# Performance work log

Hardware: AMD Instinct MI355X
Metric: run time of the kernel (lower is better)

The kernel has to match this reference:

```python
import jax, jax.numpy as jnp
import numpy as np

TEMP = 1.0
B, FLAT, K, D = 8, 262144, 256, 4  # FLAT = M*D, M = 65536


def setup_inputs() -> dict:
    key = jax.random.key(0)
    k1, k2 = jax.random.split(key)
    x = jax.random.normal(k1, (B, FLAT), dtype=jnp.float32)
    center = jax.random.normal(k2, (K, D), dtype=jnp.float32)
    return {"x": x, "center": center}


def reference(x, center):
    # Soft vector quantization (Q_type='Soft')
    x_ = x.reshape(x.shape[0], -1, D)                      # [B, M, 4]
    # sim = -||x - c||^2, expanded to avoid [B,M,K,4] intermediate
    x_sq = jnp.sum(x_ * x_, axis=-1, keepdims=True)        # [B, M, 1]
    c_sq = jnp.sum(center * center, axis=-1)               # [K]
    xc = jnp.einsum('bmd,kd->bmk', x_, center)             # [B, M, K]
    sim = -(x_sq - 2.0 * xc + c_sq)                        # [B, M, K]
    smx = jax.nn.softmax(TEMP * sim, axis=-1)              # [B, M, K]
    output = jnp.einsum('bmk,kd->bmd', smx, center)        # [B, M, 4]
    return output.reshape(x.shape)
```

## Files before the change

### kernel.cpp

```cpp
#include <hip/hip_runtime.h>
#include <hip/hip_bf16.h>

#ifndef __has_builtin
#define __has_builtin(x) 0
#endif

typedef __attribute__((ext_vector_type(8))) short short8;
typedef __attribute__((ext_vector_type(4))) float floatx4;

__device__ __forceinline__ float fast_exp2(float x) {
#if __has_builtin(__builtin_amdgcn_exp2f)
    return __builtin_amdgcn_exp2f(x);
#else
    return exp2f(x);
#endif
}
__device__ __forceinline__ float fast_rcp(float x) {
#if __has_builtin(__builtin_amdgcn_rcpf)
    return __builtin_amdgcn_rcpf(x);
#else
    return 1.0f / x;
#endif
}
__device__ __forceinline__ unsigned pack_bf16(float a, float b) {
    __hip_bfloat162 h = __float22bfloat162_rn(make_float2(a, b));
    union { __hip_bfloat162 h2; unsigned u; } cv;
    cv.h2 = h;
    return cv.u;
}

#define VQ_K 256
#define BLK  256
#define T    4

__global__ __launch_bounds__(BLK, 8) void vq_mfma(const float* __restrict__ x,
                                                  const float* __restrict__ center,
                                                  float* __restrict__ out) {
    __shared__ float    s_c2[2056];
    __shared__ float    s_b[VQ_K];
    __shared__ unsigned s_v[8 * 64 * 4];

    {
        const float L2E = 1.4426950408889634f;
        int k = threadIdx.x;
        float4 c = reinterpret_cast<const float4*>(center)[k];
        float b = -L2E * (c.x * c.x + c.y * c.y + c.z * c.z + c.w * c.w);
        int off = k * 8 + ((k >> 3) & 3) * 4;
        float s = 2.0f * L2E;
        s_c2[off + 0] = s * c.x;
        s_c2[off + 1] = s * c.y;
        s_c2[off + 2] = s * c.z;
        s_c2[off + 3] = s * c.w;
        s_b[k] = b;
    }
    for (int f = threadIdx.x; f < 512; f += BLK) {
        int chunk = f >> 6, ln = f & 63;
        int n = ln & 15, q = ln >> 4;
#pragma unroll
        for (int r = 0; r < 4; ++r) {
            int k0 = chunk * 32 + q * 8 + 2 * r;
            float v0 = (n < 4) ? center[k0 * 4 + n]       : (n == 4 ? 1.f : 0.f);
            float v1 = (n < 4) ? center[(k0 + 1) * 4 + n] : (n == 4 ? 1.f : 0.f);
            s_v[f * 4 + r] = pack_bf16(v0, v1);
        }
    }
    __syncthreads();

    const int lane = threadIdx.x & 63;
    const int wv   = threadIdx.x >> 6;
    const int q    = lane >> 4;
    const int ml   = lane & 15;

    const int mbase = blockIdx.x * (4 * 16 * T) + wv * (16 * T);
    const float4* __restrict__ x4 = reinterpret_cast<const float4*>(x);

    float4 xr[T];
#pragma unroll
    for (int t = 0; t < T; ++t) xr[t] = x4[mbase + t * 16 + ml];

    floatx4 O[T];
#pragma unroll
    for (int t = 0; t < T; ++t) O[t] = (floatx4){0.f, 0.f, 0.f, 0.f};

    union AFrag { unsigned u[4]; short8 v; };

    for (int chunk = 0; chunk < 8; ++chunk) {
        AFrag areg[T];
#pragma unroll
        for (int jj = 0; jj < 4; ++jj) {
            int k0 = chunk * 32 + q * 8 + 2 * jj;
            int o0 = k0 * 8 + q * 4;
            float4 c2a = *reinterpret_cast<const float4*>(s_c2 + o0);
            float4 c2b = *reinterpret_cast<const float4*>(s_c2 + o0 + 8);
            float  ba  = s_b[k0];
            float  bb  = s_b[k0 + 1];
#pragma unroll
            for (int t = 0; t < T; ++t) {
                float s0 = fmaf(xr[t].x, c2a.x, ba);
                s0 = fmaf(xr[t].y, c2a.y, s0);
                s0 = fmaf(xr[t].z, c2a.z, s0);
                s0 = fmaf(xr[t].w, c2a.w, s0);
                float s1 = fmaf(xr[t].x, c2b.x, bb);
                s1 = fmaf(xr[t].y, c2b.y, s1);
                s1 = fmaf(xr[t].z, c2b.z, s1);
                s1 = fmaf(xr[t].w, c2b.w, s1);
                areg[t].u[jj] = pack_bf16(fast_exp2(s0), fast_exp2(s1));
            }
        }
        short8 bfrag = reinterpret_cast<const short8*>(s_v)[chunk * 64 + lane];
#pragma unroll
        for (int t = 0; t < T; ++t) {
            O[t] = __builtin_amdgcn_mfma_f32_16x16x32_bf16(areg[t].v, bfrag,
                                                           O[t], 0, 0, 0);
        }
    }

#pragma unroll
    for (int t = 0; t < T; ++t) {
#pragma unroll
        for (int r = 0; r < 4; ++r) {
            float den = __shfl(O[t][r], (lane & 48) + 4, 64);
            float val = O[t][r] * fast_rcp(den);
            int m = mbase + t * 16 + q * 4 + r;
            if (ml < 4) out[m * 4 + ml] = val;
        }
    }
}

extern "C" void kernel_launch(void* const* d_in, const int* in_sizes, int n_in,
                              void* d_out, int out_size, void* d_ws, size_t ws_size,
                              hipStream_t stream) {
    const float* x      = (const float*)d_in[0];
    const float* center = (const float*)d_in[1];
    float* out = (float*)d_out;

    int nvec   = in_sizes[0] / 4;
    int blocks = nvec / (4 * 16 * T);
    vq_mfma<<<blocks, BLK, 0, stream>>>(x, center, out);
}
```

Before: 93.49 us.

## Compute similarity logits with split-bf16 MFMA instead of scalar FMAs

Moves the x·c + bias logit computation off the scalar FMA path and onto MFMA. x and the scaled centers are split into bf16 hi/lo pairs so the product keeps near-fp32 accuracy, with the bias folded in as a hi/lo pair against a constant-one column. The logit MFMA output feeds exp2 directly into the second MFMA's A-fragment layout, and the V layout is permuted to match. It removes about 32 VALU FMAs per logit pair but adds two extra MFMAs per tile, more setup work, and lowers the occupancy hint from 8 to 6.

```diff
diff --git a/kernel.cpp b/kernel.cpp
--- a/kernel.cpp
+++ b/kernel.cpp
@@ -22,6 +22,19 @@
     return 1.0f / x;
 #endif
 }
+__device__ __forceinline__ unsigned short bf16_of(float v) {
+    union { __hip_bfloat16 b; unsigned short s; } cv;
+    cv.b = __float2bfloat16(v);
+    return cv.s;
+}
+__device__ __forceinline__ float bf16_back(unsigned short s) {
+    union { __hip_bfloat16 b; unsigned short t; } cv;
+    cv.t = s;
+    return __bfloat162float(cv.b);
+}
+__device__ __forceinline__ unsigned bcat(unsigned short lo, unsigned short hi) {
+    return (unsigned)lo | ((unsigned)hi << 16);
+}
 __device__ __forceinline__ unsigned pack_bf16(float a, float b) {
     __hip_bfloat162 h = __float22bfloat162_rn(make_float2(a, b));
     union { __hip_bfloat162 h2; unsigned u; } cv;
@@ -33,36 +46,54 @@
 #define BLK  256
 #define T    4
 
-__global__ __launch_bounds__(BLK, 8) void vq_mfma(const float* __restrict__ x,
+__global__ __launch_bounds__(BLK, 6) void vq_mfma(const float* __restrict__ x,
                                                   const float* __restrict__ center,
                                                   float* __restrict__ out) {
-    __shared__ float    s_c2[2056];
-    __shared__ float    s_b[VQ_K];
-    __shared__ unsigned s_v[8 * 64 * 4];
+    __shared__ uint4 s_a[16 * 64];
+    __shared__ uint4 s_v[8 * 64];
 
-    {
-        const float L2E = 1.4426950408889634f;
-        int k = threadIdx.x;
+    const float L2E = 1.4426950408889634f;
+
+    for (int f = threadIdx.x; f < 1024; f += BLK) {
+        int kt = f >> 6, q = (f >> 4) & 3, ml = f & 15;
+        int k = kt * 16 + ml;
         float4 c = reinterpret_cast<const float4*>(center)[k];
+        float s = 2.0f * L2E;
+        float c2f[4] = {s * c.x, s * c.y, s * c.z, s * c.w};
+        unsigned short ch[4], cl[4];
+#pragma unroll
+        for (int d = 0; d < 4; ++d) {
+            ch[d] = bf16_of(c2f[d]);
+            cl[d] = bf16_of(c2f[d] - bf16_back(ch[d]));
+        }
         float b = -L2E * (c.x * c.x + c.y * c.y + c.z * c.z + c.w * c.w);
-        int off = k * 8 + ((k >> 3) & 3) * 4;
-        float s = 2.0f * L2E;
-        s_c2[off + 0] = s * c.x;
-        s_c2[off + 1] = s * c.y;
-        s_c2[off + 2] = s * c.z;
-        s_c2[off + 3] = s * c.w;
-        s_b[k] = b;
+        unsigned short bh = bf16_of(b);
+        unsigned short bl = bf16_of(b - bf16_back(bh));
+        uint4 e;
+        if (q == 0) {
+            e.x = bcat(ch[0], ch[1]); e.y = bcat(ch[2], ch[3]);
+            e.z = e.x;                e.w = e.y;
+        } else if (q == 1) {
+            e.x = bcat(cl[0], cl[1]); e.y = bcat(cl[2], cl[3]);
+            e.z = bcat(bh, bl);       e.w = 0;
+        } else {
+            e.x = e.y = e.z = e.w = 0;
+        }
+        s_a[f] = e;
     }
     for (int f = threadIdx.x; f < 512; f += BLK) {
-        int chunk = f >> 6, ln = f & 63;
-        int n = ln & 15, q = ln >> 4;
+        int c = f >> 6, q = (f >> 4) & 3, n = f & 15;
+        unsigned rr[4];
 #pragma unroll
         for (int r = 0; r < 4; ++r) {
-            int k0 = chunk * 32 + q * 8 + 2 * r;
-            float v0 = (n < 4) ? center[k0 * 4 + n]       : (n == 4 ? 1.f : 0.f);
-            float v1 = (n < 4) ? center[(k0 + 1) * 4 + n] : (n == 4 ? 1.f : 0.f);
-            s_v[f * 4 + r] = pack_bf16(v0, v1);
+            int j0 = 2 * r, j1 = 2 * r + 1;
+            int k0 = 32 * c + (j0 < 4 ? 4 * q + j0 : 16 + 4 * q + j0 - 4);
+            int k1 = 32 * c + (j1 < 4 ? 4 * q + j1 : 16 + 4 * q + j1 - 4);
+            float v0 = (n < 4) ? center[k0 * 4 + n] : (n == 4 ? 1.f : 0.f);
+            float v1 = (n < 4) ? center[k1 * 4 + n] : (n == 4 ? 1.f : 0.f);
+            rr[r] = bcat(bf16_of(v0), bf16_of(v1));
         }
+        s_v[f] = make_uint4(rr[0], rr[1], rr[2], rr[3]);
     }
     __syncthreads();
 
@@ -70,48 +101,52 @@
     const int wv   = threadIdx.x >> 6;
     const int q    = lane >> 4;
     const int ml   = lane & 15;
-
     const int mbase = blockIdx.x * (4 * 16 * T) + wv * (16 * T);
     const float4* __restrict__ x4 = reinterpret_cast<const float4*>(x);
 
-    float4 xr[T];
+    union Frag { uint4 u4; unsigned u[4]; short8 v; };
+
+    Frag B[T];
 #pragma unroll
-    for (int t = 0; t < T; ++t) xr[t] = x4[mbase + t * 16 + ml];
+    for (int t = 0; t < T; ++t) {
+        float4 xv = x4[mbase + t * 16 + ml];
+        unsigned short xh[4], xl[4];
+        float xf[4] = {xv.x, xv.y, xv.z, xv.w};
+#pragma unroll
+        for (int d = 0; d < 4; ++d) {
+            xh[d] = bf16_of(xf[d]);
+            xl[d] = bf16_of(xf[d] - bf16_back(xh[d]));
+        }
+        unsigned h01 = bcat(xh[0], xh[1]), h23 = bcat(xh[2], xh[3]);
+        unsigned l01 = bcat(xl[0], xl[1]), l23 = bcat(xl[2], xl[3]);
+        const unsigned ONE2 = 0x3F803F80u;
+        B[t].u[0] = (q <= 1) ? h01 : 0;
+        B[t].u[1] = (q <= 1) ? h23 : 0;
+        B[t].u[2] = (q == 0) ? l01 : ((q == 1) ? ONE2 : 0);
+        B[t].u[3] = (q == 0) ? l23 : 0;
+    }
 
     floatx4 O[T];
 #pragma unroll
     for (int t = 0; t < T; ++t) O[t] = (floatx4){0.f, 0.f, 0.f, 0.f};
 
-    union AFrag { unsigned u[4]; short8 v; };
+    const floatx4 Z4 = (floatx4){0.f, 0.f, 0.f, 0.f};
 
-    for (int chunk = 0; chunk < 8; ++chunk) {
-        AFrag areg[T];
-#pragma unroll
-        for (int jj = 0; jj < 4; ++jj) {
-            int k0 = chunk * 32 + q * 8 + 2 * jj;
-            int o0 = k0 * 8 + q * 4;
-            float4 c2a = *reinterpret_cast<const float4*>(s_c2 + o0);
-            float4 c2b = *reinterpret_cast<const float4*>(s_c2 + o0 + 8);
-            float  ba  = s_b[k0];
-            float  bb  = s_b[k0 + 1];
-#pragma unroll
-            for (int t = 0; t < T; ++t) {
-                float s0 = fmaf(xr[t].x, c2a.x, ba);
-                s0 = fmaf(xr[t].y, c2a.y, s0);
-                s0 = fmaf(xr[t].z, c2a.z, s0);
-                s0 = fmaf(xr[t].w, c2a.w, s0);
-                float s1 = fmaf(xr[t].x, c2b.x, bb);
-                s1 = fmaf(xr[t].y, c2b.y, s1);
-                s1 = fmaf(xr[t].z, c2b.z, s1);
-                s1 = fmaf(xr[t].w, c2b.w, s1);
-                areg[t].u[jj] = pack_bf16(fast_exp2(s0), fast_exp2(s1));
-            }
-        }
-        short8 bfrag = reinterpret_cast<const short8*>(s_v)[chunk * 64 + lane];
+    for (int c = 0; c < 8; ++c) {
+        Frag a0, a1, vf;
+        a0.u4 = s_a[(2 * c) * 64 + lane];
+        a1.u4 = s_a[(2 * c + 1) * 64 + lane];
+        vf.u4 = s_v[c * 64 + lane];
 #pragma unroll
         for (int t = 0; t < T; ++t) {
-            O[t] = __builtin_amdgcn_mfma_f32_16x16x32_bf16(areg[t].v, bfrag,
-                                                           O[t], 0, 0, 0);
+            floatx4 S0 = __builtin_amdgcn_mfma_f32_16x16x32_bf16(a0.v, B[t].v, Z4, 0, 0, 0);
+            floatx4 S1 = __builtin_amdgcn_mfma_f32_16x16x32_bf16(a1.v, B[t].v, Z4, 0, 0, 0);
+            Frag p;
+            p.u[0] = pack_bf16(fast_exp2(S0[0]), fast_exp2(S0[1]));
+            p.u[1] = pack_bf16(fast_exp2(S0[2]), fast_exp2(S0[3]));
+            p.u[2] = pack_bf16(fast_exp2(S1[0]), fast_exp2(S1[1]));
+            p.u[3] = pack_bf16(fast_exp2(S1[2]), fast_exp2(S1[3]));
+            O[t] = __builtin_amdgcn_mfma_f32_16x16x32_bf16(p.v, vf.v, O[t], 0, 0, 0);
         }
     }
 
```

New measurement: 84.74 us. -9.4%, faster.
